# Performance work log

Hardware: AMD Instinct MI355X
Metric: run time of the kernel (lower is better)

The kernel has to match this reference:

```python
import jax, jax.numpy as jnp
import numpy as np

N = 100_000   # nodes per type
E = 600_000   # edges per relation
D = 128       # hidden_dim
L = 2         # num_layers


def setup_inputs() -> dict:
    key = jax.random.key(0)
    ks = jax.random.split(key, 12)
    inp = {
        "x_user": jax.random.normal(ks[0], (N, D), jnp.float32),
        "x_item": jax.random.normal(ks[1], (N, D), jnp.float32),
        "ei_follows": jax.random.randint(ks[2], (2, E), 0, N, dtype=jnp.int32),  # user -> user
        "ei_rates": jax.random.randint(ks[3], (2, E), 0, N, dtype=jnp.int32),    # user -> item
    }
    i = 4
    for l in range(L):
        for rel in ("follows", "rates"):
            inp[f"W{l}_{rel}"] = (jax.random.normal(ks[i], (D, D), jnp.float32) / np.float32(np.sqrt(D)))
            inp[f"b{l}_{rel}"] = jnp.zeros((D,), jnp.float32)
            i += 1
    return inp


def _rel_conv(x_src, ei, W, b, num_dst):
    # gather src features, Linear + ReLU on messages, scatter-sum into dst
    m = jax.nn.relu(x_src[ei[0]] @ W + b)  # [E, D]
    return jax.ops.segment_sum(m, ei[1], num_segments=num_dst)  # [num_dst, D]


def reference(x_user, x_item,
              W0_follows, b0_follows, W0_rates, b0_rates,
              W1_follows, b1_follows, W1_rates, b1_rates,
              ei_follows, ei_rates):
    layers = [
        (W0_follows, b0_follows, W0_rates, b0_rates),
        (W1_follows, b1_follows, W1_rates, b1_rates),
    ]
    xu, xi = x_user, x_item
    for (Wf, bf, Wr, br) in layers:
        new_u = _rel_conv(xu, ei_follows, Wf, bf, N)  # user <- user via 'follows'
        new_i = _rel_conv(xu, ei_rates, Wr, br, N)    # item <- user via 'rates'
        xu, xi = new_u, new_i
    return xu, xi
```

## Files before the change

### kernel.cpp

```cpp
#include <hip/hip_runtime.h>

#define D 128
#define RPB_BITS 9
#define CH 8192

typedef __attribute__((ext_vector_type(8))) short bf16x8;
typedef __attribute__((ext_vector_type(4))) float f32x4;

static __device__ __forceinline__ unsigned short f2bf(float f) {
    union { float f; unsigned u; } v; v.f = f;
    unsigned r = (v.u + 0x7fffu + ((v.u >> 16) & 1u)) >> 16;
    return (unsigned short)r;
}
static __device__ __forceinline__ float bf2f(unsigned short s) {
    union { unsigned u; float f; } v; v.u = ((unsigned)s) << 16;
    return v.f;
}

static __device__ __forceinline__ void stage_W(
    const float* __restrict__ W, unsigned short* __restrict__ Wh, int w, int l)
{
    const int n = ((w & 1) << 6) + l;
    #pragma unroll
    for (int i = 0; i < 8; ++i) {
        const int k0 = ((w >> 1) << 3) + (i << 4);
        bf16x8 hv;
        #pragma unroll
        for (int j = 0; j < 8; ++j)
            hv[j] = (short)f2bf(W[(size_t)(k0 + j) * D + n]);
        *(bf16x8*)&Wh[n * D + (k0 ^ ((n & 7) << 3))] = hv;
    }
}

static __device__ __forceinline__ void stage_X(
    const float* __restrict__ X, unsigned short* Xh, unsigned short* Xl,
    int row0, int nrows, int w, int l)
{
    const int k0 = (l & 15) << 3;
    #pragma unroll
    for (int i = 0; i < 2; ++i) {
        const int r = ((w + (i << 2)) << 2) + (l >> 4);
        bf16x8 hv, lv;
        if (row0 + r < nrows) {
            const float* xp = X + (size_t)(row0 + r) * D + k0;
            #pragma unroll
            for (int j = 0; j < 8; ++j) {
                float x = xp[j];
                unsigned short h = f2bf(x);
                hv[j] = (short)h;
                lv[j] = (short)f2bf(x - bf2f(h));
            }
        } else {
            #pragma unroll
            for (int j = 0; j < 8; ++j) { hv[j] = 0; lv[j] = 0; }
        }
        const int sw = k0 ^ ((r & 7) << 3);
        *(bf16x8*)&Xh[r * D + sw] = hv;
        *(bf16x8*)&Xl[r * D + sw] = lv;
    }
}

static __device__ __forceinline__ void mfma_compute(
    const unsigned short* Xh, const unsigned short* Xl, const unsigned short* Wh,
    f32x4 acc[4], int w, int l)
{
    const int rtile = (w >> 1) << 4;
    const int c0 = (w & 1) << 6;
    const int ra = rtile + (l & 15);
    #pragma unroll
    for (int kb = 0; kb < 4; ++kb) {
        const int kk0 = (kb << 5) + ((l >> 4) << 3);
        const int swa = kk0 ^ ((ra & 7) << 3);
        const bf16x8 ah = *(const bf16x8*)&Xh[ra * D + swa];
        const bf16x8 al = *(const bf16x8*)&Xl[ra * D + swa];
        #pragma unroll
        for (int ct = 0; ct < 4; ++ct) {
            const int n = c0 + (ct << 4) + (l & 15);
            const bf16x8 bh = *(const bf16x8*)&Wh[n * D + (kk0 ^ ((n & 7) << 3))];
            acc[ct] = __builtin_amdgcn_mfma_f32_16x16x32_bf16(ah, bh, acc[ct], 0, 0, 0);
            acc[ct] = __builtin_amdgcn_mfma_f32_16x16x32_bf16(al, bh, acc[ct], 0, 0, 0);
        }
    }
}

static __device__ __forceinline__ void epilogue_store(
    const f32x4 acc[4], const float* __restrict__ bias,
    unsigned short* __restrict__ H, int row0, int nrows, int w, int l)
{
    const int rtile = (w >> 1) << 4;
    const int c0 = (w & 1) << 6;
    #pragma unroll
    for (int ct = 0; ct < 4; ++ct) {
        const int col = c0 + (ct << 4) + (l & 15);
        const float bv = bias[col];
        #pragma unroll
        for (int j = 0; j < 4; ++j) {
            const int r = row0 + rtile + ((l >> 4) << 2) + j;
            if (r < nrows)
                H[(size_t)r * D + col] = f2bf(fmaxf(acc[ct][j] + bv, 0.f));
        }
    }
}

__global__ __launch_bounds__(256) void gemm0_prehist(
    const float* __restrict__ X, const float* __restrict__ W,
    const float* __restrict__ bias, unsigned short* __restrict__ H, int nrows,
    int gemm_grid,
    const int* __restrict__ dstf, const int* __restrict__ dstr,
    int Ef, int Er, int* __restrict__ gbc)
{
    __shared__ unsigned short Xh[32 * D];
    __shared__ unsigned short Xl[32 * D];
    __shared__ unsigned short Wh[128 * D];
    __shared__ int lcnt[512];
    const int tid = threadIdx.x;
    if ((int)blockIdx.x < gemm_grid) {
        const int w = tid >> 6, l = tid & 63;
        const int row0 = blockIdx.x * 32;
        stage_W(W, Wh, w, l);
        stage_X(X, Xh, Xl, row0, nrows, w, l);
        __syncthreads();
        f32x4 acc[4] = {};
        mfma_compute(Xh, Xl, Wh, acc, w, l);
        epilogue_store(acc, bias, H, row0, nrows, w, l);
    } else {
        lcnt[tid] = 0; lcnt[tid + 256] = 0;
        __syncthreads();
        const int nb = gridDim.x - gemm_grid;
        const int bid = blockIdx.x - gemm_grid;
        const int tot = Ef + Er;
        for (int i = bid * 256 + tid; i < tot; i += nb * 256) {
            int idx = (i < Ef) ? (dstf[i] >> RPB_BITS)
                               : (256 + (dstr[i - Ef] >> RPB_BITS));
            atomicAdd(&lcnt[idx], 1);
        }
        __syncthreads();
        if (lcnt[tid])       atomicAdd(&gbc[tid],       lcnt[tid]);
        if (lcnt[tid + 256]) atomicAdd(&gbc[tid + 256], lcnt[tid + 256]);
    }
}

__global__ void scan_buckets(const int* __restrict__ gbc, int* __restrict__ gbase,
                             int* __restrict__ gcur, int* rpf_n, int* rpr_n,
                             int Ef, int Er)
{
    __shared__ int ts[256];
    const int t = threadIdx.x;
    for (int r = 0; r < 2; ++r) {
        int v = gbc[r * 256 + t];
        ts[t] = v; __syncthreads();
        int incl = v;
        for (int o = 1; o < 256; o <<= 1) {
            int y = (t >= o) ? ts[t - o] : 0;
            __syncthreads();
            incl += y; ts[t] = incl;
            __syncthreads();
        }
        gbase[r * 256 + t] = incl - v;
        gcur[r * 256 + t]  = incl - v;
        __syncthreads();
    }
    if (t == 0) { *rpf_n = Ef; *rpr_n = Er; }
}

__global__ __launch_bounds__(256) void bucket_scatter(
    const int* __restrict__ eif, const int* __restrict__ eir,
    int Ef, int Er, int chunks_f,
    int* __restrict__ gcur,
    unsigned* __restrict__ pk_f, unsigned* __restrict__ pk_r)
{
    __shared__ int cnt[256], off[256];
    const int t = threadIdx.x;
    const int cid = blockIdx.x;
    const int *src, *dst; unsigned* pk; int* cur; int base, E;
    if (cid < chunks_f) { base = cid * CH;              E = Ef; src = eif; dst = eif + Ef; pk = pk_f; cur = gcur; }
    else                { base = (cid - chunks_f) * CH; E = Er; src = eir; dst = eir + Er; pk = pk_r; cur = gcur + 256; }
    cnt[t] = 0;
    __syncthreads();
    for (int k = 0; k < CH / 256; ++k) {
        int e = base + t + k * 256;
        if (e < E) atomicAdd(&cnt[dst[e] >> RPB_BITS], 1);
    }
    __syncthreads();
    { int c = cnt[t]; if (c) off[t] = atomicAdd(&cur[t], c); }
    __syncthreads();
    for (int k = 0; k < CH / 256; ++k) {
        int e = base + t + k * 256;
        if (e < E) {
            int d = dst[e];
            int p = atomicAdd(&off[d >> RPB_BITS], 1);
            pk[p] = (unsigned)src[e] | ((unsigned)(d & 511) << 18);
        }
    }
}

__global__ __launch_bounds__(256) void csr_finalize(
    const unsigned* __restrict__ pk_f, const unsigned* __restrict__ pk_r,
    const int* __restrict__ gbase, int Ef, int Er,
    int* __restrict__ rpf, int* __restrict__ rpr,
    int* __restrict__ esf, int* __restrict__ esr, int n)
{
    __shared__ int deg[512], cur[512], ts[256];
    const int t = threadIdx.x;
    const int rel = (int)blockIdx.x >> 8;
    const int b = (int)blockIdx.x & 255;
    const unsigned* pk = rel ? pk_r : pk_f;
    int* rp = rel ? rpr : rpf;
    int* es = rel ? esr : esf;
    const int E = rel ? Er : Ef;
    const int* gb = gbase + rel * 256;
    const int beg = gb[b];
    const int end = (b == 255) ? E : gb[b + 1];
    deg[t] = 0; deg[t + 256] = 0;
    __syncthreads();
    for (int j = beg + t; j < end; j += 256)
        atomicAdd(&deg[pk[j] >> 18], 1);
    __syncthreads();
    const int a0 = deg[2 * t], a1 = deg[2 * t + 1];
    const int s = a0 + a1;
    ts[t] = s; __syncthreads();
    int incl = s;
    for (int o = 1; o < 256; o <<= 1) {
        int y = (t >= o) ? ts[t - o] : 0;
        __syncthreads();
        incl += y; ts[t] = incl;
        __syncthreads();
    }
    const int ex = incl - s;
    const int row0 = b << RPB_BITS;
    if (row0 + 2 * t < n)     rp[row0 + 2 * t]     = beg + ex;
    if (row0 + 2 * t + 1 < n) rp[row0 + 2 * t + 1] = beg + ex + a0;
    cur[2 * t] = ex; cur[2 * t + 1] = ex + a0;
    __syncthreads();
    for (int j = beg + t; j < end; j += 256) {
        unsigned v = pk[j];
        int p = atomicAdd(&cur[v >> 18], 1);
        es[beg + p] = (int)(v & 0x3ffffu);
    }
}

static __device__ __forceinline__ void segsum_row(
    const unsigned short* __restrict__ H, const int* __restrict__ rp,
    const int* __restrict__ es, float* __restrict__ out, int row, int lane16)
{
    const int c = lane16 << 3;
    float a[8] = {0.f,0.f,0.f,0.f,0.f,0.f,0.f,0.f};
    const int beg = rp[row], end = rp[row + 1];
    int sNext = (beg < end) ? es[beg] : 0;
    for (int j = beg; j < end; ++j) {
        const int s = sNext;
        sNext = (j + 1 < end) ? es[j + 1] : 0;
        const uint4 v = *(const uint4*)(H + (size_t)s * D + c);
        const unsigned dw[4] = {v.x, v.y, v.z, v.w};
        #pragma unroll
        for (int q = 0; q < 4; ++q) {
            union { unsigned u; float f; } lo, hi;
            lo.u = dw[q] << 16;
            hi.u = dw[q] & 0xffff0000u;
            a[2 * q]     += lo.f;
            a[2 * q + 1] += hi.f;
        }
    }
    float4 o0 = {a[0], a[1], a[2], a[3]};
    float4 o1 = {a[4], a[5], a[6], a[7]};
    *(float4*)(out + (size_t)row * D + c)     = o0;
    *(float4*)(out + (size_t)row * D + c + 4) = o1;
}

__global__ __launch_bounds__(256) void segsum_bf16(
    const unsigned short* __restrict__ H, const int* __restrict__ rowptr,
    const int* __restrict__ esrc, float* __restrict__ out, int nrows)
{
    const int t = blockIdx.x * 256 + threadIdx.x;
    const int row = t >> 4;
    if (row >= nrows) return;
    segsum_row(H, rowptr, esrc, out, row, t & 15);
}

__global__ __launch_bounds__(256) void segsum_bf16_dual(
    const unsigned short* __restrict__ Hf, const int* __restrict__ rpf,
    const int* __restrict__ esf, float* __restrict__ ou,
    const unsigned short* __restrict__ Hr, const int* __restrict__ rpr,
    const int* __restrict__ esr, float* __restrict__ oi,
    int nrows, int seg_grid)
{
    int bid = blockIdx.x;
    const unsigned short* H; const int* rp; const int* es; float* out;
    if (bid < seg_grid) { H = Hf; rp = rpf; es = esf; out = ou; }
    else { bid -= seg_grid; H = Hr; rp = rpr; es = esr; out = oi; }
    const int t = bid * 256 + threadIdx.x;
    const int row = t >> 4;
    if (row >= nrows) return;
    segsum_row(H, rp, es, out, row, t & 15);
}

__global__ __launch_bounds__(256) void gemm_relu_bf16_dual(
    const float* __restrict__ X,
    const float* __restrict__ W1, const float* __restrict__ b1, unsigned short* __restrict__ H1,
    const float* __restrict__ W2, const float* __restrict__ b2, unsigned short* __restrict__ H2,
    int nrows)
{
    __shared__ unsigned short Xh[32 * D];
    __shared__ unsigned short Xl[32 * D];
    __shared__ unsigned short Wh[2][128 * D];
    const int tid = threadIdx.x;
    const int w = tid >> 6, l = tid & 63;
    const int row0 = blockIdx.x * 32;
    stage_W(W1, Wh[0], w, l);
    stage_W(W2, Wh[1], w, l);
    stage_X(X, Xh, Xl, row0, nrows, w, l);
    __syncthreads();
    {
        f32x4 acc[4] = {};
        mfma_compute(Xh, Xl, Wh[0], acc, w, l);
        epilogue_store(acc, b1, H1, row0, nrows, w, l);
    }
    {
        f32x4 acc[4] = {};
        mfma_compute(Xh, Xl, Wh[1], acc, w, l);
        epilogue_store(acc, b2, H2, row0, nrows, w, l);
    }
}

static inline size_t align16(size_t x) { return (x + 15) & ~(size_t)15; }

extern "C" void kernel_launch(void* const* d_in, const int* in_sizes, int n_in,
                              void* d_out, int out_size, void* d_ws, size_t ws_size,
                              hipStream_t stream)
{
    const float* x_user = (const float*)d_in[0];
    const int*   ei_fol = (const int*)d_in[2];
    const int*   ei_rat = (const int*)d_in[3];
    const float* W0f = (const float*)d_in[4];
    const float* b0f = (const float*)d_in[5];
    const float* W1f = (const float*)d_in[8];
    const float* b1f = (const float*)d_in[9];
    const float* W1r = (const float*)d_in[10];
    const float* b1r = (const float*)d_in[11];

    const int n  = in_sizes[0] / D;
    const int Ef = in_sizes[2] / 2;
    const int Er = in_sizes[3] / 2;

    float* out_u = (float*)d_out;
    float* out_i = out_u + (size_t)n * D;
    float* U1 = out_i;

    char* ws = (char*)d_ws;
    size_t off = 0;
    unsigned short* HA = (unsigned short*)(ws + off); off = align16(off + (size_t)n * D * 2);
    unsigned short* HB = (unsigned short*)(ws + off); off = align16(off + (size_t)n * D * 2);
    int* rpf   = (int*)(ws + off); off = align16(off + (size_t)(n + 1) * 4);
    int* rpr   = (int*)(ws + off); off = align16(off + (size_t)(n + 1) * 4);
    int* esf   = (int*)(ws + off); off = align16(off + (size_t)Ef * 4);
    int* esr   = (int*)(ws + off); off = align16(off + (size_t)Er * 4);
    unsigned* pkf = (unsigned*)(ws + off); off = align16(off + (size_t)Ef * 4);
    unsigned* pkr = (unsigned*)(ws + off); off = align16(off + (size_t)Er * 4);
    int* gbc   = (int*)(ws + off); off = align16(off + 512 * 4);
    int* gbase = (int*)(ws + off); off = align16(off + 512 * 4);
    int* gcur  = (int*)(ws + off); off = align16(off + 512 * 4);
    (void)ws_size;

    const dim3 blk(256);
    const int gemm_grid = (n + 31) / 32;
    const int PB = 320;
    const int chunks_f = (Ef + CH - 1) / CH;
    const int chunks_r = (Er + CH - 1) / CH;
    const int seg_grid = (int)(((long long)n * 16 + 255) / 256);

    hipMemsetAsync(gbc, 0, 512 * sizeof(int), stream);

    gemm0_prehist<<<gemm_grid + PB, blk, 0, stream>>>(
        x_user, W0f, b0f, HA, n, gemm_grid, ei_fol + Ef, ei_rat + Er, Ef, Er, gbc);
    scan_buckets<<<1, 256, 0, stream>>>(gbc, gbase, gcur, rpf + n, rpr + n, Ef, Er);
    bucket_scatter<<<chunks_f + chunks_r, blk, 0, stream>>>(
        ei_fol, ei_rat, Ef, Er, chunks_f, gcur, pkf, pkr);
    csr_finalize<<<512, blk, 0, stream>>>(pkf, pkr, gbase, Ef, Er, rpf, rpr, esf, esr, n);

    segsum_bf16<<<seg_grid, blk, 0, stream>>>(HA, rpf, esf, U1, n);

    gemm_relu_bf16_dual<<<gemm_grid, blk, 0, stream>>>(U1, W1f, b1f, HA, W1r, b1r, HB, n);

    segsum_bf16_dual<<<2 * seg_grid, blk, 0, stream>>>(
        HA, rpf, esf, out_u, HB, rpr, esr, out_i, n, seg_grid);
}
```

Baseline: 414.9 us.

## Fuse layer-1 segment sum into dual GEMM and pre-convert weights once

Adds a small prep kernel that converts and swizzles the three weight matrices to bf16 once, so GEMM blocks copy a ready image into LDS instead of each block converting fp32 weights. The layer-0 segment sum is fused into the layer-1 dual GEMM: each block aggregates its 32 rows straight into LDS and skips the fp32 U1 round trip through global memory. A fallback path is used when the workspace is too small for a third bf16 buffer. In exchange the gather phase now uses 8 threads per row with 16 columns each, which lowers memory parallelism during aggregation, and 64KB of weight LDS per block may reduce occupancy.

```diff
diff --git a/kernel.cpp b/kernel.cpp
--- a/kernel.cpp
+++ b/kernel.cpp
@@ -17,18 +17,30 @@
     return v.f;
 }
 
-static __device__ __forceinline__ void stage_W(
-    const float* __restrict__ W, unsigned short* __restrict__ Wh, int w, int l)
-{
-    const int n = ((w & 1) << 6) + l;
+__global__ __launch_bounds__(256) void prep_w(
+    const float* __restrict__ Wa, const float* __restrict__ Wb, const float* __restrict__ Wc,
+    unsigned short* __restrict__ Ta, unsigned short* __restrict__ Tb, unsigned short* __restrict__ Tc)
+{
+    const int m = blockIdx.x >> 3;
+    const float* W = (m == 0) ? Wa : ((m == 1) ? Wb : Wc);
+    unsigned short* T = (m == 0) ? Ta : ((m == 1) ? Tb : Tc);
+    const int t = ((blockIdx.x & 7) << 8) + threadIdx.x;
+    const int n = t >> 4;
+    const int k0 = (t & 15) << 3;
+    bf16x8 hv;
+    #pragma unroll
+    for (int j = 0; j < 8; ++j)
+        hv[j] = (short)f2bf(W[(size_t)(k0 + j) * D + n]);
+    *(bf16x8*)&T[n * D + (k0 ^ ((n & 7) << 3))] = hv;
+}
+
+static __device__ __forceinline__ void stage_Wimg(
+    const unsigned short* __restrict__ Wt, unsigned short* Wh, int tid)
+{
     #pragma unroll
     for (int i = 0; i < 8; ++i) {
-        const int k0 = ((w >> 1) << 3) + (i << 4);
-        bf16x8 hv;
-        #pragma unroll
-        for (int j = 0; j < 8; ++j)
-            hv[j] = (short)f2bf(W[(size_t)(k0 + j) * D + n]);
-        *(bf16x8*)&Wh[n * D + (k0 ^ ((n & 7) << 3))] = hv;
+        const int e = (tid << 3) + (i << 11);
+        *(uint4*)&Wh[e] = *(const uint4*)&Wt[e];
     }
 }
 
@@ -103,7 +115,7 @@
 }
 
 __global__ __launch_bounds__(256) void gemm0_prehist(
-    const float* __restrict__ X, const float* __restrict__ W,
+    const float* __restrict__ X, const unsigned short* __restrict__ Wt,
     const float* __restrict__ bias, unsigned short* __restrict__ H, int nrows,
     int gemm_grid,
     const int* __restrict__ dstf, const int* __restrict__ dstr,
@@ -117,7 +129,7 @@
     if ((int)blockIdx.x < gemm_grid) {
         const int w = tid >> 6, l = tid & 63;
         const int row0 = blockIdx.x * 32;
-        stage_W(W, Wh, w, l);
+        stage_Wimg(Wt, Wh, tid);
         stage_X(X, Xh, Xl, row0, nrows, w, l);
         __syncthreads();
         f32x4 acc[4] = {};
@@ -236,6 +248,83 @@
         unsigned v = pk[j];
         int p = atomicAdd(&cur[v >> 18], 1);
         es[beg + p] = (int)(v & 0x3ffffu);
+    }
+}
+
+__global__ __launch_bounds__(256) void seg_dualgemm(
+    const unsigned short* __restrict__ H0,
+    const int* __restrict__ rp, const int* __restrict__ es,
+    const unsigned short* __restrict__ Wt1, const float* __restrict__ b1,
+    unsigned short* __restrict__ H1,
+    const unsigned short* __restrict__ Wt2, const float* __restrict__ b2,
+    unsigned short* __restrict__ H2,
+    float* __restrict__ U1out, int nrows)
+{
+    __shared__ unsigned short Xh[32 * D];
+    __shared__ unsigned short Xl[32 * D];
+    __shared__ unsigned short Wh[2][128 * D];
+    const int tid = threadIdx.x;
+    const int row0 = blockIdx.x * 32;
+
+    stage_Wimg(Wt1, Wh[0], tid);
+    if (Wt2) stage_Wimg(Wt2, Wh[1], tid);
+
+    const int rl = tid >> 3;
+    const int r = row0 + rl;
+    const int c0 = (tid & 7) << 4;
+    float a[16];
+    #pragma unroll
+    for (int q = 0; q < 16; ++q) a[q] = 0.f;
+    if (r < nrows) {
+        const int beg = rp[r], end = rp[r + 1];
+        for (int j = beg; j < end; ++j) {
+            const unsigned short* hp = H0 + (size_t)es[j] * D + c0;
+            const uint4 v0 = *(const uint4*)hp;
+            const uint4 v1 = *(const uint4*)(hp + 8);
+            const unsigned dw[8] = {v0.x, v0.y, v0.z, v0.w, v1.x, v1.y, v1.z, v1.w};
+            #pragma unroll
+            for (int q = 0; q < 8; ++q) {
+                union { unsigned u; float f; } lo, hi;
+                lo.u = dw[q] << 16; hi.u = dw[q] & 0xffff0000u;
+                a[2 * q]     += lo.f;
+                a[2 * q + 1] += hi.f;
+            }
+        }
+        if (U1out) {
+            float4* up = (float4*)(U1out + (size_t)r * D + c0);
+            up[0] = make_float4(a[0], a[1], a[2], a[3]);
+            up[1] = make_float4(a[4], a[5], a[6], a[7]);
+            up[2] = make_float4(a[8], a[9], a[10], a[11]);
+            up[3] = make_float4(a[12], a[13], a[14], a[15]);
+        }
+    }
+
+    bf16x8 hv0, lv0, hv1, lv1;
+    #pragma unroll
+    for (int q = 0; q < 8; ++q) {
+        unsigned short h0 = f2bf(a[q]);
+        hv0[q] = (short)h0; lv0[q] = (short)f2bf(a[q] - bf2f(h0));
+        unsigned short h1 = f2bf(a[q + 8]);
+        hv1[q] = (short)h1; lv1[q] = (short)f2bf(a[q + 8] - bf2f(h1));
+    }
+    const int sw0 = c0 ^ ((rl & 7) << 3);
+    const int sw1 = (c0 + 8) ^ ((rl & 7) << 3);
+    *(bf16x8*)&Xh[rl * D + sw0] = hv0;
+    *(bf16x8*)&Xl[rl * D + sw0] = lv0;
+    *(bf16x8*)&Xh[rl * D + sw1] = hv1;
+    *(bf16x8*)&Xl[rl * D + sw1] = lv1;
+    __syncthreads();
+
+    const int w = tid >> 6, l = tid & 63;
+    {
+        f32x4 acc[4] = {};
+        mfma_compute(Xh, Xl, Wh[0], acc, w, l);
+        epilogue_store(acc, b1, H1, row0, nrows, w, l);
+    }
+    if (Wt2) {
+        f32x4 acc[4] = {};
+        mfma_compute(Xh, Xl, Wh[1], acc, w, l);
+        epilogue_store(acc, b2, H2, row0, nrows, w, l);
     }
 }
 
@@ -267,16 +356,6 @@
     *(float4*)(out + (size_t)row * D + c + 4) = o1;
 }
 
-__global__ __launch_bounds__(256) void segsum_bf16(
-    const unsigned short* __restrict__ H, const int* __restrict__ rowptr,
-    const int* __restrict__ esrc, float* __restrict__ out, int nrows)
-{
-    const int t = blockIdx.x * 256 + threadIdx.x;
-    const int row = t >> 4;
-    if (row >= nrows) return;
-    segsum_row(H, rowptr, esrc, out, row, t & 15);
-}
-
 __global__ __launch_bounds__(256) void segsum_bf16_dual(
     const unsigned short* __restrict__ Hf, const int* __restrict__ rpf,
     const int* __restrict__ esf, float* __restrict__ ou,
@@ -292,34 +371,6 @@
     const int row = t >> 4;
     if (row >= nrows) return;
     segsum_row(H, rp, es, out, row, t & 15);
-}
-
-__global__ __launch_bounds__(256) void gemm_relu_bf16_dual(
-    const float* __restrict__ X,
-    const float* __restrict__ W1, const float* __restrict__ b1, unsigned short* __restrict__ H1,
-    const float* __restrict__ W2, const float* __restrict__ b2, unsigned short* __restrict__ H2,
-    int nrows)
-{
-    __shared__ unsigned short Xh[32 * D];
-    __shared__ unsigned short Xl[32 * D];
-    __shared__ unsigned short Wh[2][128 * D];
-    const int tid = threadIdx.x;
-    const int w = tid >> 6, l = tid & 63;
-    const int row0 = blockIdx.x * 32;
-    stage_W(W1, Wh[0], w, l);
-    stage_W(W2, Wh[1], w, l);
-    stage_X(X, Xh, Xl, row0, nrows, w, l);
-    __syncthreads();
-    {
-        f32x4 acc[4] = {};
-        mfma_compute(Xh, Xl, Wh[0], acc, w, l);
-        epilogue_store(acc, b1, H1, row0, nrows, w, l);
-    }
-    {
-        f32x4 acc[4] = {};
-        mfma_compute(Xh, Xl, Wh[1], acc, w, l);
-        epilogue_store(acc, b2, H2, row0, nrows, w, l);
-    }
 }
 
 static inline size_t align16(size_t x) { return (x + 15) & ~(size_t)15; }
@@ -344,7 +395,6 @@
 
     float* out_u = (float*)d_out;
     float* out_i = out_u + (size_t)n * D;
-    float* U1 = out_i;
 
     char* ws = (char*)d_ws;
     size_t off = 0;
@@ -356,10 +406,14 @@
     int* esr   = (int*)(ws + off); off = align16(off + (size_t)Er * 4);
     unsigned* pkf = (unsigned*)(ws + off); off = align16(off + (size_t)Ef * 4);
     unsigned* pkr = (unsigned*)(ws + off); off = align16(off + (size_t)Er * 4);
+    unsigned short* Wt0 = (unsigned short*)(ws + off); off = align16(off + (size_t)D * D * 2);
+    unsigned short* Wt1 = (unsigned short*)(ws + off); off = align16(off + (size_t)D * D * 2);
+    unsigned short* Wt2 = (unsigned short*)(ws + off); off = align16(off + (size_t)D * D * 2);
     int* gbc   = (int*)(ws + off); off = align16(off + 512 * 4);
     int* gbase = (int*)(ws + off); off = align16(off + 512 * 4);
     int* gcur  = (int*)(ws + off); off = align16(off + 512 * 4);
-    (void)ws_size;
+    unsigned short* HC = (unsigned short*)(ws + off);
+    const bool big = (off + (size_t)n * D * 2) <= ws_size;
 
     const dim3 blk(256);
     const int gemm_grid = (n + 31) / 32;
@@ -369,18 +423,26 @@
     const int seg_grid = (int)(((long long)n * 16 + 255) / 256);
 
     hipMemsetAsync(gbc, 0, 512 * sizeof(int), stream);
+    prep_w<<<24, blk, 0, stream>>>(W0f, W1f, W1r, Wt0, Wt1, Wt2);
 
     gemm0_prehist<<<gemm_grid + PB, blk, 0, stream>>>(
-        x_user, W0f, b0f, HA, n, gemm_grid, ei_fol + Ef, ei_rat + Er, Ef, Er, gbc);
+        x_user, Wt0, b0f, HA, n, gemm_grid, ei_fol + Ef, ei_rat + Er, Ef, Er, gbc);
     scan_buckets<<<1, 256, 0, stream>>>(gbc, gbase, gcur, rpf + n, rpr + n, Ef, Er);
     bucket_scatter<<<chunks_f + chunks_r, blk, 0, stream>>>(
         ei_fol, ei_rat, Ef, Er, chunks_f, gcur, pkf, pkr);
     csr_finalize<<<512, blk, 0, stream>>>(pkf, pkr, gbase, Ef, Er, rpf, rpr, esf, esr, n);
 
-    segsum_bf16<<<seg_grid, blk, 0, stream>>>(HA, rpf, esf, U1, n);
-
-    gemm_relu_bf16_dual<<<gemm_grid, blk, 0, stream>>>(U1, W1f, b1f, HA, W1r, b1r, HB, n);
-
-    segsum_bf16_dual<<<2 * seg_grid, blk, 0, stream>>>(
-        HA, rpf, esf, out_u, HB, rpr, esr, out_i, n, seg_grid);
-}
+    if (big) {
+        seg_dualgemm<<<gemm_grid, blk, 0, stream>>>(
+            HA, rpf, esf, Wt1, b1f, HB, Wt2, b1r, HC, nullptr, n);
+        segsum_bf16_dual<<<2 * seg_grid, blk, 0, stream>>>(
+            HB, rpf, esf, out_u, HC, rpr, esr, out_i, n, seg_grid);
+    } else {
+        seg_dualgemm<<<gemm_grid, blk, 0, stream>>>(
+            HA, rpf, esf, Wt1, b1f, HB, nullptr, nullptr, nullptr, out_i, n);
+        gemm0_prehist<<<gemm_grid, blk, 0, stream>>>(
+            out_i, Wt2, b1r, HA, n, gemm_grid, ei_fol + Ef, ei_rat + Er, Ef, Er, gbc);
+        segsum_bf16_dual<<<2 * seg_grid, blk, 0, stream>>>(
+            HB, rpf, esf, out_u, HA, rpr, esr, out_i, n, seg_grid);
+    }
+}
```

After: 428.5 us. 3.3% more time.
